# Optimization experiments

Hardware: AMD Instinct MI355X
Metric: run time of the kernel (lower is better)

Reference implementation:

```python
import jax, jax.numpy as jnp
import numpy as np

N_ENTITIES = 100000
N_EDGES = 1250000
N_RELATIONS = 32
D = 64


def setup_inputs() -> dict:
    key = jax.random.key(0)
    k1, k2, k3, k4 = jax.random.split(key, 4)
    entity_emb = jax.random.normal(k1, (N_ENTITIES, D), dtype=jnp.float32)
    edge_index = jax.random.randint(k2, (2, N_EDGES), 0, N_ENTITIES, dtype=jnp.int64)
    edge_type = jax.random.randint(k3, (N_EDGES,), 0, N_RELATIONS, dtype=jnp.int64)
    weight = jax.random.normal(k4, (N_RELATIONS, D), dtype=jnp.float32)
    return {"entity_emb": entity_emb, "edge_index": edge_index,
            "edge_type": edge_type, "weight": weight}


def reference(entity_emb, edge_index, edge_type, weight):
    n_entities = entity_emb.shape[0]
    head, tail = edge_index[0], edge_index[1]
    # gather tail entity embeddings and relation embeddings, elementwise multiply
    neigh_relation_emb = entity_emb[tail] * weight[edge_type]  # [E, D]
    # scatter_mean by head index
    sums = jax.ops.segment_sum(neigh_relation_emb, head, num_segments=n_entities)
    counts = jax.ops.segment_sum(jnp.ones((head.shape[0],), dtype=entity_emb.dtype),
                                 head, num_segments=n_entities)
    entity_agg = sums / jnp.maximum(counts, 1.0)[:, None]  # empty segments -> 0
    return entity_agg
```

## Files before the change

kernel.cpp:

```cpp
#include <hip/hip_runtime.h>

#define D 64
#define BIN_SHIFT 7
#define BIN_SIZE 128
#define MAX_BINS 1024
#define BINCAP 2560
#define K1_THREADS 512
#define K1_EPT 10
#define K1_EPB (K1_THREADS * K1_EPT)
#define K2_THREADS 512
#define NREL 32


__device__ __forceinline__ float bf2f(unsigned short u) {
    union { unsigned i; float f; } x; x.i = ((unsigned)u) << 16; return x.f;
}

__global__ void cvt_kernel(const float* __restrict__ emb,
                           unsigned short* __restrict__ emb16,
                           int* __restrict__ binCount, int nbins, long n4) {
    long i = (long)blockIdx.x * blockDim.x + threadIdx.x;
    if (i < (long)nbins) binCount[i] = 0;
    if (i >= n4) return;
    float4 v = ((const float4*)emb)[i];
    ushort4 o;
    unsigned b;
    b = __float_as_uint(v.x); o.x = (unsigned short)((b + 0x7FFF + ((b >> 16) & 1)) >> 16);
    b = __float_as_uint(v.y); o.y = (unsigned short)((b + 0x7FFF + ((b >> 16) & 1)) >> 16);
    b = __float_as_uint(v.z); o.z = (unsigned short)((b + 0x7FFF + ((b >> 16) & 1)) >> 16);
    b = __float_as_uint(v.w); o.w = (unsigned short)((b + 0x7FFF + ((b >> 16) & 1)) >> 16);
    ((ushort4*)emb16)[i] = o;
}

__global__ void __launch_bounds__(K1_THREADS)
bin_sort_kernel(const int* __restrict__ head,
                const int* __restrict__ tail,
                const int* __restrict__ etype,
                int* __restrict__ binCount,
                unsigned* __restrict__ recs,
                int nbins, int n_edges) {
    __shared__ unsigned srec[K1_EPB];
    __shared__ int hist[MAX_BINS];
    __shared__ int base[MAX_BINS + 1];
    __shared__ int cur[MAX_BINS];
    __shared__ int gpos[MAX_BINS];
    __shared__ int tmp[K1_THREADS];
    __shared__ unsigned short binof[K1_EPB];

    int tid = threadIdx.x;
    for (int b = tid; b < MAX_BINS; b += K1_THREADS) hist[b] = 0;
    __syncthreads();

    long blockBase = (long)blockIdx.x * K1_EPB;
    int nvalid = (int)(((long)n_edges - blockBase < (long)K1_EPB)
                       ? ((long)n_edges - blockBase) : (long)K1_EPB);

    unsigned rv[K1_EPT]; int bv[K1_EPT];
#pragma unroll
    for (int k = 0; k < K1_EPT; k++) {
        long e = blockBase + (long)k * K1_THREADS + tid;
        if (e < n_edges) {
            int h = head[e];
            bv[k] = h >> BIN_SHIFT;
            rv[k] = (unsigned)tail[e] | ((unsigned)etype[e] << 17)
                  | ((unsigned)(h & (BIN_SIZE - 1)) << 22);
            atomicAdd(&hist[bv[k]], 1);
        } else bv[k] = -1;
    }
    __syncthreads();

    int s0 = hist[2 * tid], s1 = hist[2 * tid + 1];
    tmp[tid] = s0 + s1;
    __syncthreads();
    for (int s = 1; s < K1_THREADS; s <<= 1) {
        int x = (tid >= s) ? tmp[tid - s] : 0;
        __syncthreads();
        tmp[tid] += x;
        __syncthreads();
    }
    int pairExcl = tmp[tid] - (s0 + s1);
    base[2 * tid] = pairExcl;          cur[2 * tid] = pairExcl;
    base[2 * tid + 1] = pairExcl + s0; cur[2 * tid + 1] = pairExcl + s0;
    if (tid == K1_THREADS - 1) base[MAX_BINS] = tmp[tid];
    __syncthreads();

    for (int b = tid; b < nbins; b += K1_THREADS) {
        int c = hist[b];
        gpos[b] = (c > 0) ? atomicAdd(&binCount[b], c) : 0;
    }
    __syncthreads();

#pragma unroll
    for (int k = 0; k < K1_EPT; k++) {
        if (bv[k] >= 0) {
            int p = atomicAdd(&cur[bv[k]], 1);
            srec[p] = rv[k];
        }
    }
    __syncthreads();

    for (int b = tid; b < nbins; b += K1_THREADS) {
        int j0 = base[b], j1 = base[b + 1];
        for (int j = j0; j < j1; j++) binof[j] = (unsigned short)b;
    }
    __syncthreads();

    for (int i = tid; i < nvalid; i += K1_THREADS) {
        int b = binof[i];
        int off = gpos[b] + (i - base[b]);
        if (off < BINCAP)
            recs[(long)b * BINCAP + off] = srec[i];
    }
}

__global__ void __launch_bounds__(K2_THREADS, 2)
aggregate_bin_kernel(const unsigned short* __restrict__ emb16,
                     const float* __restrict__ weight,
                     const unsigned* __restrict__ recs,
                     const int* __restrict__ binCount,
                     float* __restrict__ out, int n_ent) {
    __shared__ unsigned raw[BINCAP];
    __shared__ unsigned sorted[BINCAP + 16];
    __shared__ float wlds[NREL * D];
    __shared__ int hist[BIN_SIZE];
    __shared__ int off[BIN_SIZE];
    __shared__ int cur[BIN_SIZE];

    int tid = threadIdx.x;
    int b = blockIdx.x;
    int n = min(binCount[b], BINCAP);

    if (tid < 16) sorted[n + tid] = 0u;
    for (int i = tid; i < NREL * D; i += K2_THREADS) wlds[i] = weight[i];
    if (tid < BIN_SIZE) hist[tid] = 0;
    __syncthreads();

    const unsigned* gr = recs + (long)b * BINCAP;
    for (int i = tid; i < n; i += K2_THREADS) {
        unsigned q = gr[i];
        raw[i] = q;
        atomicAdd(&hist[(q >> 22) & 127], 1);
    }
    __syncthreads();

    int lane = tid & 63;
    int wave = tid >> 6;

    if (wave == 0) {
        int h0 = hist[lane];
        int h1 = hist[64 + lane];
        int s0 = h0, s1 = h1;
#pragma unroll
        for (int s = 1; s < 64; s <<= 1) {
            int t0 = __shfl_up(s0, s);
            int t1 = __shfl_up(s1, s);
            if (lane >= s) { s0 += t0; s1 += t1; }
        }
        int tot0 = __shfl(s0, 63);
        int e0 = s0 - h0;
        int e1 = tot0 + s1 - h1;
        off[lane] = e0;      cur[lane] = e0;
        off[64 + lane] = e1; cur[64 + lane] = e1;
    }
    __syncthreads();

    for (int i = tid; i < n; i += K2_THREADS) {
        unsigned q = raw[i];
        int p = atomicAdd(&cur[(q >> 22) & 127], 1);
        sorted[p] = q;
    }
    __syncthreads();

    int g = lane >> 4;
    int c4 = (lane & 15) << 2;
    int hbase = b << BIN_SHIFT;

    int oA, dA, oB, dB;
    unsigned qa0, qa1, qa2, qa3, qb0, qb1, qb2, qb3;
    ushort4 ua0, ua1, ua2, ua3, ub0, ub1, ub2, ub3;
    float4 wa0, wa1, wa2, wa3, wb0, wb1, wb2, wb3;

#define K2_PREF(J, o_, d_, q0, q1, q2, q3, u0, u1, u2, u3, w0, w1, w2, w3)    \
    do {                                                                       \
        int hh_ = wave + ((J) << 3);                                           \
        o_ = off[hh_]; d_ = hist[hh_];                                         \
        q0 = sorted[o_ + g];      q1 = sorted[o_ + 4 + g];                     \
        q2 = sorted[o_ + 8 + g];  q3 = sorted[o_ + 12 + g];                    \
        q0 = (g < d_)      ? q0 : 0u;                                          \
        q1 = (4 + g < d_)  ? q1 : 0u;                                          \
        q2 = (8 + g < d_)  ? q2 : 0u;                                          \
        q3 = (12 + g < d_) ? q3 : 0u;                                          \
        u0 = *(const ushort4*)&emb16[((long)(q0 & 0x1FFFF) << 6) + c4];        \
        u1 = *(const ushort4*)&emb16[((long)(q1 & 0x1FFFF) << 6) + c4];        \
        u2 = *(const ushort4*)&emb16[((long)(q2 & 0x1FFFF) << 6) + c4];        \
        u3 = *(const ushort4*)&emb16[((long)(q3 & 0x1FFFF) << 6) + c4];        \
        w0 = *(const float4*)&wlds[(((q0 >> 17) & 31) << 6) + c4];             \
        w1 = *(const float4*)&wlds[(((q1 >> 17) & 31) << 6) + c4];             \
        w2 = *(const float4*)&wlds[(((q2 >> 17) & 31) << 6) + c4];             \
        w3 = *(const float4*)&wlds[(((q3 >> 17) & 31) << 6) + c4];             \
    } while (0)

#define K2_COMP(J, o_, d_, q0, q1, q2, q3, u0, u1, u2, u3, w0, w1, w2, w3)    \
    do {                                                                       \
        int hh_ = wave + ((J) << 3);                                           \
        float4 acc = make_float4(0.f, 0.f, 0.f, 0.f);                          \
        float m0 = (g < d_)      ? 1.f : 0.f;                                  \
        float m1 = (4 + g < d_)  ? 1.f : 0.f;                                  \
        float m2 = (8 + g < d_)  ? 1.f : 0.f;                                  \
        float m3 = (12 + g < d_) ? 1.f : 0.f;                                  \
        acc.x += m0 * bf2f(u0.x) * w0.x; acc.y += m0 * bf2f(u0.y) * w0.y;      \
        acc.z += m0 * bf2f(u0.z) * w0.z; acc.w += m0 * bf2f(u0.w) * w0.w;      \
        acc.x += m1 * bf2f(u1.x) * w1.x; acc.y += m1 * bf2f(u1.y) * w1.y;      \
        acc.z += m1 * bf2f(u1.z) * w1.z; acc.w += m1 * bf2f(u1.w) * w1.w;      \
        acc.x += m2 * bf2f(u2.x) * w2.x; acc.y += m2 * bf2f(u2.y) * w2.y;      \
        acc.z += m2 * bf2f(u2.z) * w2.z; acc.w += m2 * bf2f(u2.w) * w2.w;      \
        acc.x += m3 * bf2f(u3.x) * w3.x; acc.y += m3 * bf2f(u3.y) * w3.y;      \
        acc.z += m3 * bf2f(u3.z) * w3.z; acc.w += m3 * bf2f(u3.w) * w3.w;      \
        for (int i_ = 16; i_ < d_; i_ += 16) {          \
            int e0_ = i_ + g, e1_ = i_ + 4 + g, e2_ = i_ + 8 + g,              \
                e3_ = i_ + 12 + g;                                             \
            unsigned t0 = sorted[o_ + e0_]; unsigned t1 = sorted[o_ + e1_];    \
            unsigned t2 = sorted[o_ + e2_]; unsigned t3 = sorted[o_ + e3_];    \
            t0 = (e0_ < d_) ? t0 : 0u;  t1 = (e1_ < d_) ? t1 : 0u;             \
            t2 = (e2_ < d_) ? t2 : 0u;  t3 = (e3_ < d_) ? t3 : 0u;             \
            ushort4 v0 = *(const ushort4*)&emb16[((long)(t0 & 0x1FFFF) << 6) + c4]; \
            ushort4 v1 = *(const ushort4*)&emb16[((long)(t1 & 0x1FFFF) << 6) + c4]; \
            ushort4 v2 = *(const ushort4*)&emb16[((long)(t2 & 0x1FFFF) << 6) + c4]; \
            ushort4 v3 = *(const ushort4*)&emb16[((long)(t3 & 0x1FFFF) << 6) + c4]; \
            float4 x0 = *(const float4*)&wlds[(((t0 >> 17) & 31) << 6) + c4];  \
            float4 x1 = *(const float4*)&wlds[(((t1 >> 17) & 31) << 6) + c4];  \
            float4 x2 = *(const float4*)&wlds[(((t2 >> 17) & 31) << 6) + c4];  \
            float4 x3 = *(const float4*)&wlds[(((t3 >> 17) & 31) << 6) + c4];  \
            float n0 = (e0_ < d_) ? 1.f : 0.f;                                 \
            float n1 = (e1_ < d_) ? 1.f : 0.f;                                 \
            float n2 = (e2_ < d_) ? 1.f : 0.f;                                 \
            float n3 = (e3_ < d_) ? 1.f : 0.f;                                 \
            acc.x += n0 * bf2f(v0.x) * x0.x; acc.y += n0 * bf2f(v0.y) * x0.y;  \
            acc.z += n0 * bf2f(v0.z) * x0.z; acc.w += n0 * bf2f(v0.w) * x0.w;  \
            acc.x += n1 * bf2f(v1.x) * x1.x; acc.y += n1 * bf2f(v1.y) * x1.y;  \
            acc.z += n1 * bf2f(v1.z) * x1.z; acc.w += n1 * bf2f(v1.w) * x1.w;  \
            acc.x += n2 * bf2f(v2.x) * x2.x; acc.y += n2 * bf2f(v2.y) * x2.y;  \
            acc.z += n2 * bf2f(v2.z) * x2.z; acc.w += n2 * bf2f(v2.w) * x2.w;  \
            acc.x += n3 * bf2f(v3.x) * x3.x; acc.y += n3 * bf2f(v3.y) * x3.y;  \
            acc.z += n3 * bf2f(v3.z) * x3.z; acc.w += n3 * bf2f(v3.w) * x3.w;  \
        }                                                                      \
        acc.x += __shfl_xor(acc.x, 16); acc.y += __shfl_xor(acc.y, 16);        \
        acc.z += __shfl_xor(acc.z, 16); acc.w += __shfl_xor(acc.w, 16);        \
        acc.x += __shfl_xor(acc.x, 32); acc.y += __shfl_xor(acc.y, 32);        \
        acc.z += __shfl_xor(acc.z, 32); acc.w += __shfl_xor(acc.w, 32);        \
        if (g == 0 && hbase + hh_ < n_ent) {                                   \
            float inv = 1.f / fmaxf((float)d_, 1.f);                           \
            *(float4*)&out[((long)(hbase + hh_) << 6) + c4] =                  \
                make_float4(acc.x * inv, acc.y * inv, acc.z * inv, acc.w * inv);\
        }                                                                      \
    } while (0)

    K2_PREF(0, oA, dA, qa0, qa1, qa2, qa3, ua0, ua1, ua2, ua3, wa0, wa1, wa2, wa3);
#pragma unroll 1
    for (int j = 0; j < 16; j += 2) {
        K2_PREF(j + 1, oB, dB, qb0, qb1, qb2, qb3, ub0, ub1, ub2, ub3,
                wb0, wb1, wb2, wb3);
        K2_COMP(j, oA, dA, qa0, qa1, qa2, qa3, ua0, ua1, ua2, ua3,
                wa0, wa1, wa2, wa3);
        int jn = (j + 2 < 16) ? (j + 2) : 15;
        K2_PREF(jn, oA, dA, qa0, qa1, qa2, qa3, ua0, ua1, ua2, ua3,
                wa0, wa1, wa2, wa3);
        K2_COMP(j + 1, oB, dB, qb0, qb1, qb2, qb3, ub0, ub1, ub2, ub3,
                wb0, wb1, wb2, wb3);
    }
#undef K2_PREF
#undef K2_COMP
}

__global__ void fb_scatter(const float* __restrict__ emb, const int* __restrict__ head,
                           const int* __restrict__ tail, const int* __restrict__ etype,
                           const float* __restrict__ weight, float* __restrict__ out,
                           float* __restrict__ cnt, int n_edges) {
    int gtid = blockIdx.x * blockDim.x + threadIdx.x;
    int e = gtid >> 6, lane = threadIdx.x & 63;
    if (e >= n_edges) return;
    int h = head[e], t = tail[e], r = etype[e];
    atomicAdd(&out[(long)h * D + lane], emb[(long)t * D + lane] * weight[r * D + lane]);
    if (lane == 0) atomicAdd(&cnt[h], 1.0f);
}
__global__ void fb_divide(float* __restrict__ out, const float* __restrict__ cnt, int n) {
    int i = blockIdx.x * blockDim.x + threadIdx.x;
    if (i < n) out[i] = out[i] / fmaxf(cnt[i >> 6], 1.0f);
}


extern "C" void kernel_launch(void* const* d_in, const int* in_sizes, int n_in,
                              void* d_out, int out_size, void* d_ws, size_t ws_size,
                              hipStream_t stream) {
    const float* emb    = (const float*)d_in[0];
    const int*   eidx   = (const int*)  d_in[1];
    const int*   etype  = (const int*)  d_in[2];
    const float* weight = (const float*)d_in[3];
    float* out = (float*)d_out;

    int n_edges = in_sizes[2];
    int n_ent   = out_size / D;
    const int* head = eidx;
    const int* tail = eidx + n_edges;

    int nbins = (n_ent + BIN_SIZE - 1) >> BIN_SHIFT;
    size_t recs_bytes = sizeof(int) * ((size_t)nbins * BINCAP);
    size_t cnt_bytes  = sizeof(int) * (size_t)nbins;
    size_t emb16_off  = (cnt_bytes + recs_bytes + 15) & ~((size_t)15);
    size_t need = emb16_off + (size_t)n_ent * D * sizeof(unsigned short);
    long mean_load = (n_ent > 0) ? ((long)n_edges * BIN_SIZE / n_ent) : 0;
    bool ok = (n_ent <= 131072) && (nbins <= MAX_BINS) && (ws_size >= need) &&
              (mean_load + 700 <= BINCAP);

    if (ok) {
        int* binCount  = (int*)d_ws;
        unsigned* recs = (unsigned*)(binCount + nbins);
        unsigned short* emb16 = (unsigned short*)((char*)d_ws + emb16_off);

        long n4 = (long)n_ent * D / 4;
        cvt_kernel<<<(int)((n4 + 255) / 256), 256, 0, stream>>>(
            emb, emb16, binCount, nbins, n4);

        int nblocks = (n_edges + K1_EPB - 1) / K1_EPB;
        bin_sort_kernel<<<nblocks, K1_THREADS, 0, stream>>>(
            head, tail, etype, binCount, recs, nbins, n_edges);

        aggregate_bin_kernel<<<nbins, K2_THREADS, 0, stream>>>(
            emb16, weight, recs, binCount, out, n_ent);
    } else {
        float* cnt = (float*)d_ws;
        hipMemsetAsync(out, 0, (size_t)out_size * sizeof(float), stream);
        hipMemsetAsync(cnt, 0, (size_t)n_ent * sizeof(float), stream);
        long tt = (long)n_edges * 64;
        fb_scatter<<<(int)((tt + 255) / 256), 256, 0, stream>>>(
            emb, head, tail, etype, weight, out, cnt, n_edges);
        fb_divide<<<(out_size + 255) / 256, 256, 0, stream>>>(out, cnt, out_size);
    }
}
```

Before: 146.7 us.

## Scatter bin records directly to global using per-bin atomic rank

The binning kernel drops its shared-memory local sort (prefix scan, staging buffer, bin-of table). Each edge's rank within its bin now comes from the shared atomic counter and is written straight to global memory. The block size is also halved to 256 threads, giving more blocks with less LDS each. This removes the scan and several barriers, but the global writes are no longer contiguous per bin, so coalescing becomes worse.

```diff
diff --git a/kernel.cpp b/kernel.cpp
--- a/kernel.cpp
+++ b/kernel.cpp
@@ -5,7 +5,7 @@
 #define BIN_SIZE 128
 #define MAX_BINS 1024
 #define BINCAP 2560
-#define K1_THREADS 512
+#define K1_THREADS 256
 #define K1_EPT 10
 #define K1_EPB (K1_THREADS * K1_EPT)
 #define K2_THREADS 512
@@ -39,23 +39,16 @@
                 int* __restrict__ binCount,
                 unsigned* __restrict__ recs,
                 int nbins, int n_edges) {
-    __shared__ unsigned srec[K1_EPB];
-    __shared__ int hist[MAX_BINS];
-    __shared__ int base[MAX_BINS + 1];
-    __shared__ int cur[MAX_BINS];
+    __shared__ int cnt[MAX_BINS];
     __shared__ int gpos[MAX_BINS];
-    __shared__ int tmp[K1_THREADS];
-    __shared__ unsigned short binof[K1_EPB];
 
     int tid = threadIdx.x;
-    for (int b = tid; b < MAX_BINS; b += K1_THREADS) hist[b] = 0;
+    for (int b = tid; b < nbins; b += K1_THREADS) cnt[b] = 0;
     __syncthreads();
 
     long blockBase = (long)blockIdx.x * K1_EPB;
-    int nvalid = (int)(((long)n_edges - blockBase < (long)K1_EPB)
-                       ? ((long)n_edges - blockBase) : (long)K1_EPB);
-
-    unsigned rv[K1_EPT]; int bv[K1_EPT];
+
+    unsigned rv[K1_EPT]; int bv[K1_EPT]; int rk[K1_EPT];
 #pragma unroll
     for (int k = 0; k < K1_EPT; k++) {
         long e = blockBase + (long)k * K1_THREADS + tid;
@@ -64,28 +57,13 @@
             bv[k] = h >> BIN_SHIFT;
             rv[k] = (unsigned)tail[e] | ((unsigned)etype[e] << 17)
                   | ((unsigned)(h & (BIN_SIZE - 1)) << 22);
-            atomicAdd(&hist[bv[k]], 1);
+            rk[k] = atomicAdd(&cnt[bv[k]], 1);
         } else bv[k] = -1;
     }
     __syncthreads();
 
-    int s0 = hist[2 * tid], s1 = hist[2 * tid + 1];
-    tmp[tid] = s0 + s1;
-    __syncthreads();
-    for (int s = 1; s < K1_THREADS; s <<= 1) {
-        int x = (tid >= s) ? tmp[tid - s] : 0;
-        __syncthreads();
-        tmp[tid] += x;
-        __syncthreads();
-    }
-    int pairExcl = tmp[tid] - (s0 + s1);
-    base[2 * tid] = pairExcl;          cur[2 * tid] = pairExcl;
-    base[2 * tid + 1] = pairExcl + s0; cur[2 * tid + 1] = pairExcl + s0;
-    if (tid == K1_THREADS - 1) base[MAX_BINS] = tmp[tid];
-    __syncthreads();
-
     for (int b = tid; b < nbins; b += K1_THREADS) {
-        int c = hist[b];
+        int c = cnt[b];
         gpos[b] = (c > 0) ? atomicAdd(&binCount[b], c) : 0;
     }
     __syncthreads();
@@ -93,23 +71,10 @@
 #pragma unroll
     for (int k = 0; k < K1_EPT; k++) {
         if (bv[k] >= 0) {
-            int p = atomicAdd(&cur[bv[k]], 1);
-            srec[p] = rv[k];
+            int dst = gpos[bv[k]] + rk[k];
+            if (dst < BINCAP)
+                recs[(long)bv[k] * BINCAP + dst] = rv[k];
         }
-    }
-    __syncthreads();
-
-    for (int b = tid; b < nbins; b += K1_THREADS) {
-        int j0 = base[b], j1 = base[b + 1];
-        for (int j = j0; j < j1; j++) binof[j] = (unsigned short)b;
-    }
-    __syncthreads();
-
-    for (int i = tid; i < nvalid; i += K1_THREADS) {
-        int b = binof[i];
-        int off = gpos[b] + (i - base[b]);
-        if (off < BINCAP)
-            recs[(long)b * BINCAP + off] = srec[i];
     }
 }
 
```

Result: slower. 155.8 us (+6.2%).
